# Kernel tuning notes

Measured on AMD Instinct MI355X. Metric: run time of the kernel, lower is better.

The kernel has to match this reference:

```python
import jax, jax.numpy as jnp
import numpy as np

IN_DIM = 50
N_Y = 100
HID = 256
STEPS = 100
BATCH = 16384


def setup_inputs() -> dict:
    key = jax.random.key(0)
    ks = jax.random.split(key, 12)
    def lin(k, out_d, in_d):
        bound = 1.0 / np.sqrt(in_d)
        return jax.random.uniform(k, (out_d, in_d), jnp.float32, -bound, bound)
    def vec(k, out_d, in_d):
        bound = 1.0 / np.sqrt(in_d)
        return jax.random.uniform(k, (out_d,), jnp.float32, -bound, bound)
    return {
        "x": jax.random.normal(ks[0], (BATCH, IN_DIM), jnp.float32),
        "W1": lin(ks[1], 128, IN_DIM), "b1": vec(ks[2], 128, IN_DIM),
        "W2": lin(ks[3], 128, 128), "b2": vec(ks[4], 128, 128),
        "W3": lin(ks[5], HID, 128), "b3": vec(ks[6], HID, 128),
        "Wih": lin(ks[7], 4 * HID, HID), "Whh": lin(ks[8], 4 * HID, HID),
        "bih": vec(ks[9], 4 * HID, HID), "bhh": vec(ks[10], 4 * HID, HID),
        "Wo": lin(ks[11], N_Y, HID),
        "bo": vec(jax.random.fold_in(key, 99), N_Y, HID),
    }


def _forward(x, W1, b1, W2, b2, W3, b3, Wih, Whh, bih, bhh, Wo, bo):
    h = jax.nn.relu(x @ W1.T + b1)
    h = jax.nn.relu(h @ W2.T + b2)
    h = jax.nn.relu(h @ W3.T + b3)  # [B, 256] -> h0 and c0
    # LSTMCell input is h itself, so x@Wih.T + h@Whh.T == h @ (Wih+Whh).T
    Wg = (Wih + Whh).T            # [256, 1024]
    bg = bih + bhh                # [1024]

    def step(carry, _):
        ht, ct = carry
        gates = ht @ Wg + bg                       # [B, 1024]
        i, f, g, o = jnp.split(gates, 4, axis=-1)  # PyTorch gate order i,f,g,o
        i = jax.nn.sigmoid(i)
        f = jax.nn.sigmoid(f)
        g = jnp.tanh(g)
        o = jax.nn.sigmoid(o)
        ct = f * ct + i * g
        ht = o * jnp.tanh(ct)
        y = ht @ Wo.T + bo                         # [B, n_y]
        return (ht, ct), y

    (_, _), ys = jax.lax.scan(step, (h, h), None, length=STEPS)
    return jnp.transpose(ys, (1, 0, 2))  # [B, STEPS, n_y]


def reference(x, W1, b1, W2, b2, W3, b3, Wih, Whh, bih, bhh, Wo, bo):
    return _forward(x, W1, b1, W2, b2, W3, b3, Wih, Whh, bih, bhh, Wo, bo)
```

## Files before the change

### kernel.cpp

```cpp
#include <hip/hip_runtime.h>

#define IN_DIM 50
#define H1 128
#define H2 128
#define HID 256
#define NGATE 1024
#define N_Y 100
#define NYP 128
#define STEPS 100
#define BATCH 16384
#define ROWS 64
#define NTHR 512

typedef float f32x16 __attribute__((ext_vector_type(16)));
typedef __bf16 bf16x8 __attribute__((ext_vector_type(8)));
typedef int i32x4 __attribute__((ext_vector_type(4)));

#define CSTRIDE 264
#define HHI_OFF 0
#define HLO_OFF 33792
#define H2T_OFF 67584
#define SMEM_BYTES 100352

#define WGH_OFF 0
#define WGL_OFF 524288
#define WOH_OFF 1048576
#define WOL_OFF 1114112
#define BG_OFF  1179648
#define BO_OFF  1183744

__device__ __forceinline__ float fast_sigmoid(float x) {
    float e = __expf(-x);
    return __builtin_amdgcn_rcpf(1.0f + e);
}
__device__ __forceinline__ float fast_tanh(float x) {
    float e = __expf(2.0f * x);
    return 1.0f - 2.0f * __builtin_amdgcn_rcpf(1.0f + e);
}
__device__ __forceinline__ unsigned short bf16bits(float x) {
    __bf16 b = (__bf16)x;
    return __builtin_bit_cast(unsigned short, b);
}
__device__ __forceinline__ float bits2f(unsigned short u) {
    __bf16 b = __builtin_bit_cast(__bf16, u);
    return (float)b;
}
__device__ __forceinline__ f32x16 splat16(float v) {
    f32x16 r;
    #pragma unroll
    for (int i = 0; i < 16; ++i) r[i] = v;
    return r;
}

extern "C" __global__ void prep_kernel(const float* __restrict__ Wih,
                                       const float* __restrict__ Whh,
                                       const float* __restrict__ bih,
                                       const float* __restrict__ bhh,
                                       const float* __restrict__ Wo,
                                       const float* __restrict__ bo,
                                       char* __restrict__ ws) {
    int idx = blockIdx.x * blockDim.x + threadIdx.x;
    if (idx < 262144) {
        int n = idx >> 8, k = idx & 255;
        float v = Wih[n * HID + k] + Whh[n * HID + k];
        __bf16 hi = (__bf16)v;
        __bf16 lo = (__bf16)(v - (float)hi);
        int dst = ((n >> 5) * 16 + (k >> 4)) * 512 + ((n & 31) + 32 * ((k >> 3) & 1)) * 8 + (k & 7);
        ((__bf16*)(ws + WGH_OFF))[dst] = hi;
        ((__bf16*)(ws + WGL_OFF))[dst] = lo;
    } else if (idx < 294912) {
        int j = idx - 262144;
        int n = j >> 8, k = j & 255;
        float v = (n < N_Y) ? Wo[n * HID + k] : 0.0f;
        __bf16 hi = (__bf16)v;
        __bf16 lo = (__bf16)(v - (float)hi);
        int dst = ((n >> 5) * 16 + (k >> 4)) * 512 + ((n & 31) + 32 * ((k >> 3) & 1)) * 8 + (k & 7);
        ((__bf16*)(ws + WOH_OFF))[dst] = hi;
        ((__bf16*)(ws + WOL_OFF))[dst] = lo;
    } else if (idx < 295936) {
        int n = idx - 294912;
        ((float*)(ws + BG_OFF))[n] = bih[n] + bhh[n];
    } else if (idx < 296064) {
        int n = idx - 295936;
        ((float*)(ws + BO_OFF))[n] = (n < N_Y) ? bo[n] : 0.0f;
    }
}

extern "C" __global__ void __launch_bounds__(NTHR, 2)
rnn_main(const float* __restrict__ x,
         const float* __restrict__ W1, const float* __restrict__ b1,
         const float* __restrict__ W2, const float* __restrict__ b2,
         const float* __restrict__ W3, const float* __restrict__ b3,
         const char* __restrict__ ws,
         float* __restrict__ out)
{
    __shared__ __align__(16) char smem[SMEM_BYTES];

    const int tid  = threadIdx.x;
    const int lane = tid & 63;
    const int lm   = lane & 31;
    const int l5   = lane >> 5;
    const int w    = __builtin_amdgcn_readfirstlane(tid >> 6);
    const int r0   = blockIdx.x * ROWS;

    {
        float* xt  = (float*)(smem + HHI_OFF);
        float* h1t = (float*)(smem + HLO_OFF);
        float* h2t = (float*)(smem + H2T_OFF);

        for (int i = tid; i < ROWS * IN_DIM; i += NTHR) {
            int r = i / IN_DIM, k = i - r * IN_DIM;
            xt[k * ROWS + r] = x[(size_t)(r0 + r) * IN_DIM + k];
        }
        __syncthreads();

        #pragma unroll
        for (int jt = 0; jt < 2; ++jt) {
            const int jb = w * 16 + jt * 8;
            float acc[8];
            #pragma unroll
            for (int jj = 0; jj < 8; ++jj) acc[jj] = b1[jb + jj];
            for (int k = 0; k < IN_DIM; ++k) {
                float h = xt[k * ROWS + lane];
                #pragma unroll
                for (int jj = 0; jj < 8; ++jj)
                    acc[jj] = fmaf(h, W1[(jb + jj) * IN_DIM + k], acc[jj]);
            }
            #pragma unroll
            for (int jj = 0; jj < 8; ++jj)
                h1t[(jb + jj) * ROWS + lane] = fmaxf(acc[jj], 0.0f);
        }
        __syncthreads();

        #pragma unroll
        for (int jt = 0; jt < 2; ++jt) {
            const int jb = w * 16 + jt * 8;
            float acc[8];
            #pragma unroll
            for (int jj = 0; jj < 8; ++jj) acc[jj] = b2[jb + jj];
            for (int k = 0; k < H1; ++k) {
                float h = h1t[k * ROWS + lane];
                #pragma unroll
                for (int jj = 0; jj < 8; ++jj)
                    acc[jj] = fmaf(h, W2[(jb + jj) * H1 + k], acc[jj]);
            }
            #pragma unroll
            for (int jj = 0; jj < 8; ++jj)
                h2t[(jb + jj) * ROWS + lane] = fmaxf(acc[jj], 0.0f);
        }
        __syncthreads();

        unsigned short* hhi = (unsigned short*)(smem + HHI_OFF);
        unsigned short* hlo = (unsigned short*)(smem + HLO_OFF);
        #pragma unroll
        for (int jt = 0; jt < 4; ++jt) {
            const int jb = w * 32 + jt * 8;
            float acc[8];
            #pragma unroll
            for (int jj = 0; jj < 8; ++jj) acc[jj] = b3[jb + jj];
            for (int k = 0; k < H2; ++k) {
                float h = h2t[k * ROWS + lane];
                #pragma unroll
                for (int jj = 0; jj < 8; ++jj)
                    acc[jj] = fmaf(h, W3[(jb + jj) * H2 + k], acc[jj]);
            }
            #pragma unroll
            for (int jj = 0; jj < 8; ++jj) {
                float v = fmaxf(acc[jj], 0.0f);
                unsigned short hb = bf16bits(v);
                unsigned short lb = bf16bits(v - bits2f(hb));
                hhi[lane * CSTRIDE + jb + jj] = hb;
                hlo[lane * CSTRIDE + jb + jj] = lb;
            }
        }
        __syncthreads();
    }

    const bf16x8* __restrict__ BgH = (const bf16x8*)(ws + WGH_OFF);
    const bf16x8* __restrict__ BgL = (const bf16x8*)(ws + WGL_OFF);
    const bf16x8* __restrict__ BoH = (const bf16x8*)(ws + WOH_OFF);
    const bf16x8* __restrict__ BoL = (const bf16x8*)(ws + WOL_OFF);
    const float*  __restrict__ bg  = (const float*)(ws + BG_OFF);
    const float*  __restrict__ boP = (const float*)(ws + BO_OFF);

    float bgv[4];
    #pragma unroll
    for (int c = 0; c < 4; ++c) bgv[c] = bg[c * 256 + w * 32 + lm];
    const int yct = w & 3, yrt = w >> 2;
    const float bo_v = boP[yct * 32 + lm];

    const int aoff = lm * (CSTRIDE * 2) + l5 * 16;
    const int colb = (w * 32 + lm) * 2;

    float cst[2][16];
    {
        const unsigned short* hhi = (const unsigned short*)(smem + HHI_OFF);
        const unsigned short* hlo = (const unsigned short*)(smem + HLO_OFF);
        #pragma unroll
        for (int rt = 0; rt < 2; ++rt)
            #pragma unroll
            for (int r = 0; r < 16; ++r) {
                int row = rt * 32 + (r & 3) + 8 * (r >> 2) + 4 * l5;
                int cell = w * 32 + lm;
                cst[rt][r] = bits2f(hhi[row * CSTRIDE + cell]) + bits2f(hlo[row * CSTRIDE + cell]);
            }
    }

    for (int t = 0; t < STEPS; ++t) {
        f32x16 acc[4][2];
        #pragma unroll
        for (int c = 0; c < 4; ++c) {
            acc[c][0] = splat16(bgv[c]);
            acc[c][1] = splat16(bgv[c]);
        }

        #pragma unroll 2
        for (int kk = 0; kk < 16; ++kk) {
            const int kb = kk * 32;
            bf16x8 ah0 = __builtin_bit_cast(bf16x8, *(const i32x4*)(smem + HHI_OFF + aoff + kb));
            bf16x8 ah1 = __builtin_bit_cast(bf16x8, *(const i32x4*)(smem + HHI_OFF + 16896 + aoff + kb));
            bf16x8 al0 = __builtin_bit_cast(bf16x8, *(const i32x4*)(smem + HLO_OFF + aoff + kb));
            bf16x8 al1 = __builtin_bit_cast(bf16x8, *(const i32x4*)(smem + HLO_OFF + 16896 + aoff + kb));
            #pragma unroll
            for (int c = 0; c < 4; ++c) {
                const int fb = ((c * 8 + w) * 16 + kk) * 64 + lane;
                bf16x8 bh = BgH[fb];
                bf16x8 bl = BgL[fb];
                acc[c][0] = __builtin_amdgcn_mfma_f32_32x32x16_bf16(ah0, bh, acc[c][0], 0, 0, 0);
                acc[c][1] = __builtin_amdgcn_mfma_f32_32x32x16_bf16(ah1, bh, acc[c][1], 0, 0, 0);
                acc[c][0] = __builtin_amdgcn_mfma_f32_32x32x16_bf16(al0, bh, acc[c][0], 0, 0, 0);
                acc[c][1] = __builtin_amdgcn_mfma_f32_32x32x16_bf16(al1, bh, acc[c][1], 0, 0, 0);
                acc[c][0] = __builtin_amdgcn_mfma_f32_32x32x16_bf16(ah0, bl, acc[c][0], 0, 0, 0);
                acc[c][1] = __builtin_amdgcn_mfma_f32_32x32x16_bf16(ah1, bl, acc[c][1], 0, 0, 0);
            }
        }

        unsigned int hn[2][16];
        #pragma unroll
        for (int rt = 0; rt < 2; ++rt)
            #pragma unroll
            for (int r = 0; r < 16; ++r) {
                float vi = fast_sigmoid(acc[0][rt][r]);
                float vf = fast_sigmoid(acc[1][rt][r]);
                float vg = fast_tanh(acc[2][rt][r]);
                float vo = fast_sigmoid(acc[3][rt][r]);
                float c  = fmaf(vf, cst[rt][r], vi * vg);
                cst[rt][r] = c;
                float h  = vo * fast_tanh(c);
                unsigned short hb = bf16bits(h);
                unsigned short lb = bf16bits(h - bits2f(hb));
                hn[rt][r] = (unsigned int)hb | ((unsigned int)lb << 16);
            }

        __syncthreads();

        #pragma unroll
        for (int rt = 0; rt < 2; ++rt)
            #pragma unroll
            for (int r = 0; r < 16; ++r) {
                int row = rt * 32 + (r & 3) + 8 * (r >> 2) + 4 * l5;
                int ro = row * (CSTRIDE * 2) + colb;
                *(unsigned short*)(smem + HHI_OFF + ro) = (unsigned short)hn[rt][r];
                *(unsigned short*)(smem + HLO_OFF + ro) = (unsigned short)(hn[rt][r] >> 16);
            }

        __syncthreads();

        f32x16 ya = splat16(bo_v);
        const int yao = yrt * 16896 + aoff;
        #pragma unroll 2
        for (int kk = 0; kk < 16; ++kk) {
            const int kb = kk * 32;
            bf16x8 ah = __builtin_bit_cast(bf16x8, *(const i32x4*)(smem + HHI_OFF + yao + kb));
            bf16x8 al = __builtin_bit_cast(bf16x8, *(const i32x4*)(smem + HLO_OFF + yao + kb));
            const int fb = (yct * 16 + kk) * 64 + lane;
            bf16x8 bh = BoH[fb];
            bf16x8 bl = BoL[fb];
            ya = __builtin_amdgcn_mfma_f32_32x32x16_bf16(ah, bh, ya, 0, 0, 0);
            ya = __builtin_amdgcn_mfma_f32_32x32x16_bf16(al, bh, ya, 0, 0, 0);
            ya = __builtin_amdgcn_mfma_f32_32x32x16_bf16(ah, bl, ya, 0, 0, 0);
        }
        const int col = yct * 32 + lm;
        if (col < N_Y) {
            #pragma unroll
            for (int r = 0; r < 16; ++r) {
                int row = yrt * 32 + (r & 3) + 8 * (r >> 2) + 4 * l5;
                out[(size_t)(r0 + row) * (STEPS * N_Y) + t * N_Y + col] = ya[r];
            }
        }
    }
}

extern "C" void kernel_launch(void* const* d_in, const int* in_sizes, int n_in,
                              void* d_out, int out_size, void* d_ws, size_t ws_size,
                              hipStream_t stream) {
    const float* x   = (const float*)d_in[0];
    const float* W1  = (const float*)d_in[1];
    const float* b1  = (const float*)d_in[2];
    const float* W2  = (const float*)d_in[3];
    const float* b2  = (const float*)d_in[4];
    const float* W3  = (const float*)d_in[5];
    const float* b3  = (const float*)d_in[6];
    const float* Wih = (const float*)d_in[7];
    const float* Whh = (const float*)d_in[8];
    const float* bih = (const float*)d_in[9];
    const float* bhh = (const float*)d_in[10];
    const float* Wo  = (const float*)d_in[11];
    const float* bo  = (const float*)d_in[12];
    float* out = (float*)d_out;
    char* ws = (char*)d_ws;

    hipLaunchKernelGGL(prep_kernel, dim3(1157), dim3(256), 0, stream,
                       Wih, Whh, bih, bhh, Wo, bo, ws);
    hipLaunchKernelGGL(rnn_main, dim3(BATCH / ROWS), dim3(NTHR), 0, stream,
                       x, W1, b1, W2, b2, W3, b3, ws, out);
}
```

Baseline: 3.501 ms.

## Split LSTM gate tiles across 16 waves with shared-memory i*g exchange

Doubles the block to 1024 threads so each wave computes two gate tiles instead of four. The lower eight waves compute i and g, store i*g to a new shared-memory exchange buffer, and later run the output projection. The upper eight waves compute f and o, update the cell state and write the new h. The aim is to halve per-wave accumulator registers and MFMA work on the recurrent critical path. In exchange it uses more shared memory (133 KB per block), adds a barrier and a cross-wave data exchange, and leaves half the waves idle during the elementwise update.

```diff
diff --git a/kernel.cpp b/kernel.cpp
--- a/kernel.cpp
+++ b/kernel.cpp
@@ -4,13 +4,11 @@
 #define H1 128
 #define H2 128
 #define HID 256
-#define NGATE 1024
 #define N_Y 100
-#define NYP 128
 #define STEPS 100
 #define BATCH 16384
 #define ROWS 64
-#define NTHR 512
+#define NTHR 1024
 
 typedef float f32x16 __attribute__((ext_vector_type(16)));
 typedef __bf16 bf16x8 __attribute__((ext_vector_type(8)));
@@ -19,8 +17,11 @@
 #define CSTRIDE 264
 #define HHI_OFF 0
 #define HLO_OFF 33792
-#define H2T_OFF 67584
-#define SMEM_BYTES 100352
+#define EXCH_OFF 67584
+#define SMEM_BYTES 133120
+#define H1T_OFF 0
+#define XT_OFF  67584
+#define H2T_OFF 80384
 
 #define WGH_OFF 0
 #define WGL_OFF 524288
@@ -86,7 +87,7 @@
     }
 }
 
-extern "C" __global__ void __launch_bounds__(NTHR, 2)
+extern "C" __global__ void __launch_bounds__(NTHR, 4)
 rnn_main(const float* __restrict__ x,
          const float* __restrict__ W1, const float* __restrict__ b1,
          const float* __restrict__ W2, const float* __restrict__ b2,
@@ -102,10 +103,14 @@
     const int l5   = lane >> 5;
     const int w    = __builtin_amdgcn_readfirstlane(tid >> 6);
     const int r0   = blockIdx.x * ROWS;
+    const bool isLo = (w < 8);
+    const int cb   = w & 7;
+    const int nt0  = (isLo ? 0 : 8) + cb;
+    const int nt1  = nt0 + 16;
 
     {
-        float* xt  = (float*)(smem + HHI_OFF);
-        float* h1t = (float*)(smem + HLO_OFF);
+        float* xt  = (float*)(smem + XT_OFF);
+        float* h1t = (float*)(smem + H1T_OFF);
         float* h2t = (float*)(smem + H2T_OFF);
 
         for (int i = tid; i < ROWS * IN_DIM; i += NTHR) {
@@ -114,47 +119,45 @@
         }
         __syncthreads();
 
+        {
+            const int jb = w * 8;
+            float acc[8];
+            #pragma unroll
+            for (int jj = 0; jj < 8; ++jj) acc[jj] = b1[jb + jj];
+            for (int k = 0; k < IN_DIM; ++k) {
+                float h = xt[k * ROWS + lane];
+                #pragma unroll
+                for (int jj = 0; jj < 8; ++jj)
+                    acc[jj] = fmaf(h, W1[(jb + jj) * IN_DIM + k], acc[jj]);
+            }
+            #pragma unroll
+            for (int jj = 0; jj < 8; ++jj)
+                h1t[(jb + jj) * ROWS + lane] = fmaxf(acc[jj], 0.0f);
+        }
+        __syncthreads();
+
+        {
+            const int jb = w * 8;
+            float acc[8];
+            #pragma unroll
+            for (int jj = 0; jj < 8; ++jj) acc[jj] = b2[jb + jj];
+            for (int k = 0; k < H1; ++k) {
+                float h = h1t[k * ROWS + lane];
+                #pragma unroll
+                for (int jj = 0; jj < 8; ++jj)
+                    acc[jj] = fmaf(h, W2[(jb + jj) * H1 + k], acc[jj]);
+            }
+            #pragma unroll
+            for (int jj = 0; jj < 8; ++jj)
+                h2t[(jb + jj) * ROWS + lane] = fmaxf(acc[jj], 0.0f);
+        }
+        __syncthreads();
+
+        unsigned short* hhi = (unsigned short*)(smem + HHI_OFF);
+        unsigned short* hlo = (unsigned short*)(smem + HLO_OFF);
         #pragma unroll
         for (int jt = 0; jt < 2; ++jt) {
             const int jb = w * 16 + jt * 8;
-            float acc[8];
-            #pragma unroll
-            for (int jj = 0; jj < 8; ++jj) acc[jj] = b1[jb + jj];
-            for (int k = 0; k < IN_DIM; ++k) {
-                float h = xt[k * ROWS + lane];
-                #pragma unroll
-                for (int jj = 0; jj < 8; ++jj)
-                    acc[jj] = fmaf(h, W1[(jb + jj) * IN_DIM + k], acc[jj]);
-            }
-            #pragma unroll
-            for (int jj = 0; jj < 8; ++jj)
-                h1t[(jb + jj) * ROWS + lane] = fmaxf(acc[jj], 0.0f);
-        }
-        __syncthreads();
-
-        #pragma unroll
-        for (int jt = 0; jt < 2; ++jt) {
-            const int jb = w * 16 + jt * 8;
-            float acc[8];
-            #pragma unroll
-            for (int jj = 0; jj < 8; ++jj) acc[jj] = b2[jb + jj];
-            for (int k = 0; k < H1; ++k) {
-                float h = h1t[k * ROWS + lane];
-                #pragma unroll
-                for (int jj = 0; jj < 8; ++jj)
-                    acc[jj] = fmaf(h, W2[(jb + jj) * H1 + k], acc[jj]);
-            }
-            #pragma unroll
-            for (int jj = 0; jj < 8; ++jj)
-                h2t[(jb + jj) * ROWS + lane] = fmaxf(acc[jj], 0.0f);
-        }
-        __syncthreads();
-
-        unsigned short* hhi = (unsigned short*)(smem + HHI_OFF);
-        unsigned short* hlo = (unsigned short*)(smem + HLO_OFF);
-        #pragma unroll
-        for (int jt = 0; jt < 4; ++jt) {
-            const int jb = w * 32 + jt * 8;
             float acc[8];
             #pragma unroll
             for (int jj = 0; jj < 8; ++jj) acc[jj] = b3[jb + jj];
@@ -183,17 +186,18 @@
     const float*  __restrict__ bg  = (const float*)(ws + BG_OFF);
     const float*  __restrict__ boP = (const float*)(ws + BO_OFF);
 
-    float bgv[4];
-    #pragma unroll
-    for (int c = 0; c < 4; ++c) bgv[c] = bg[c * 256 + w * 32 + lm];
-    const int yct = w & 3, yrt = w >> 2;
+    const float bg0 = bg[nt0 * 32 + lm];
+    const float bg1 = bg[nt1 * 32 + lm];
+    const int yrt = w >> 2, yct = w & 3;
     const float bo_v = boP[yct * 32 + lm];
 
     const int aoff = lm * (CSTRIDE * 2) + l5 * 16;
-    const int colb = (w * 32 + lm) * 2;
+    const int colb = (cb * 32 + lm) * 2;
+    float* exch = (float*)(smem + EXCH_OFF);
+    const int exbase = (cb * 2 * 16) * 64 + lane;
 
     float cst[2][16];
-    {
+    if (!isLo) {
         const unsigned short* hhi = (const unsigned short*)(smem + HHI_OFF);
         const unsigned short* hlo = (const unsigned short*)(smem + HLO_OFF);
         #pragma unroll
@@ -201,18 +205,15 @@
             #pragma unroll
             for (int r = 0; r < 16; ++r) {
                 int row = rt * 32 + (r & 3) + 8 * (r >> 2) + 4 * l5;
-                int cell = w * 32 + lm;
+                int cell = cb * 32 + lm;
                 cst[rt][r] = bits2f(hhi[row * CSTRIDE + cell]) + bits2f(hlo[row * CSTRIDE + cell]);
             }
     }
 
     for (int t = 0; t < STEPS; ++t) {
-        f32x16 acc[4][2];
-        #pragma unroll
-        for (int c = 0; c < 4; ++c) {
-            acc[c][0] = splat16(bgv[c]);
-            acc[c][1] = splat16(bgv[c]);
-        }
+        f32x16 g0[2], g1[2];
+        g0[0] = splat16(bg0); g0[1] = splat16(bg0);
+        g1[0] = splat16(bg1); g1[1] = splat16(bg1);
 
         #pragma unroll 2
         for (int kk = 0; kk < 16; ++kk) {
@@ -221,71 +222,78 @@
             bf16x8 ah1 = __builtin_bit_cast(bf16x8, *(const i32x4*)(smem + HHI_OFF + 16896 + aoff + kb));
             bf16x8 al0 = __builtin_bit_cast(bf16x8, *(const i32x4*)(smem + HLO_OFF + aoff + kb));
             bf16x8 al1 = __builtin_bit_cast(bf16x8, *(const i32x4*)(smem + HLO_OFF + 16896 + aoff + kb));
-            #pragma unroll
-            for (int c = 0; c < 4; ++c) {
-                const int fb = ((c * 8 + w) * 16 + kk) * 64 + lane;
-                bf16x8 bh = BgH[fb];
-                bf16x8 bl = BgL[fb];
-                acc[c][0] = __builtin_amdgcn_mfma_f32_32x32x16_bf16(ah0, bh, acc[c][0], 0, 0, 0);
-                acc[c][1] = __builtin_amdgcn_mfma_f32_32x32x16_bf16(ah1, bh, acc[c][1], 0, 0, 0);
-                acc[c][0] = __builtin_amdgcn_mfma_f32_32x32x16_bf16(al0, bh, acc[c][0], 0, 0, 0);
-                acc[c][1] = __builtin_amdgcn_mfma_f32_32x32x16_bf16(al1, bh, acc[c][1], 0, 0, 0);
-                acc[c][0] = __builtin_amdgcn_mfma_f32_32x32x16_bf16(ah0, bl, acc[c][0], 0, 0, 0);
-                acc[c][1] = __builtin_amdgcn_mfma_f32_32x32x16_bf16(ah1, bl, acc[c][1], 0, 0, 0);
-            }
-        }
-
-        unsigned int hn[2][16];
-        #pragma unroll
-        for (int rt = 0; rt < 2; ++rt)
-            #pragma unroll
-            for (int r = 0; r < 16; ++r) {
-                float vi = fast_sigmoid(acc[0][rt][r]);
-                float vf = fast_sigmoid(acc[1][rt][r]);
-                float vg = fast_tanh(acc[2][rt][r]);
-                float vo = fast_sigmoid(acc[3][rt][r]);
-                float c  = fmaf(vf, cst[rt][r], vi * vg);
-                cst[rt][r] = c;
-                float h  = vo * fast_tanh(c);
-                unsigned short hb = bf16bits(h);
-                unsigned short lb = bf16bits(h - bits2f(hb));
-                hn[rt][r] = (unsigned int)hb | ((unsigned int)lb << 16);
-            }
-
-        __syncthreads();
-
-        #pragma unroll
-        for (int rt = 0; rt < 2; ++rt)
-            #pragma unroll
-            for (int r = 0; r < 16; ++r) {
-                int row = rt * 32 + (r & 3) + 8 * (r >> 2) + 4 * l5;
-                int ro = row * (CSTRIDE * 2) + colb;
-                *(unsigned short*)(smem + HHI_OFF + ro) = (unsigned short)hn[rt][r];
-                *(unsigned short*)(smem + HLO_OFF + ro) = (unsigned short)(hn[rt][r] >> 16);
-            }
-
-        __syncthreads();
-
-        f32x16 ya = splat16(bo_v);
-        const int yao = yrt * 16896 + aoff;
-        #pragma unroll 2
-        for (int kk = 0; kk < 16; ++kk) {
-            const int kb = kk * 32;
-            bf16x8 ah = __builtin_bit_cast(bf16x8, *(const i32x4*)(smem + HHI_OFF + yao + kb));
-            bf16x8 al = __builtin_bit_cast(bf16x8, *(const i32x4*)(smem + HLO_OFF + yao + kb));
-            const int fb = (yct * 16 + kk) * 64 + lane;
-            bf16x8 bh = BoH[fb];
-            bf16x8 bl = BoL[fb];
-            ya = __builtin_amdgcn_mfma_f32_32x32x16_bf16(ah, bh, ya, 0, 0, 0);
-            ya = __builtin_amdgcn_mfma_f32_32x32x16_bf16(al, bh, ya, 0, 0, 0);
-            ya = __builtin_amdgcn_mfma_f32_32x32x16_bf16(ah, bl, ya, 0, 0, 0);
-        }
-        const int col = yct * 32 + lm;
-        if (col < N_Y) {
-            #pragma unroll
-            for (int r = 0; r < 16; ++r) {
-                int row = yrt * 32 + (r & 3) + 8 * (r >> 2) + 4 * l5;
-                out[(size_t)(r0 + row) * (STEPS * N_Y) + t * N_Y + col] = ya[r];
+            bf16x8 b0h = BgH[(nt0 * 16 + kk) * 64 + lane];
+            bf16x8 b0l = BgL[(nt0 * 16 + kk) * 64 + lane];
+            bf16x8 b1h = BgH[(nt1 * 16 + kk) * 64 + lane];
+            bf16x8 b1l = BgL[(nt1 * 16 + kk) * 64 + lane];
+            g0[0] = __builtin_amdgcn_mfma_f32_32x32x16_bf16(ah0, b0h, g0[0], 0, 0, 0);
+            g0[1] = __builtin_amdgcn_mfma_f32_32x32x16_bf16(ah1, b0h, g0[1], 0, 0, 0);
+            g0[0] = __builtin_amdgcn_mfma_f32_32x32x16_bf16(al0, b0h, g0[0], 0, 0, 0);
+            g0[1] = __builtin_amdgcn_mfma_f32_32x32x16_bf16(al1, b0h, g0[1], 0, 0, 0);
+            g0[0] = __builtin_amdgcn_mfma_f32_32x32x16_bf16(ah0, b0l, g0[0], 0, 0, 0);
+            g0[1] = __builtin_amdgcn_mfma_f32_32x32x16_bf16(ah1, b0l, g0[1], 0, 0, 0);
+            g1[0] = __builtin_amdgcn_mfma_f32_32x32x16_bf16(ah0, b1h, g1[0], 0, 0, 0);
+            g1[1] = __builtin_amdgcn_mfma_f32_32x32x16_bf16(ah1, b1h, g1[1], 0, 0, 0);
+            g1[0] = __builtin_amdgcn_mfma_f32_32x32x16_bf16(al0, b1h, g1[0], 0, 0, 0);
+            g1[1] = __builtin_amdgcn_mfma_f32_32x32x16_bf16(al1, b1h, g1[1], 0, 0, 0);
+            g1[0] = __builtin_amdgcn_mfma_f32_32x32x16_bf16(ah0, b1l, g1[0], 0, 0, 0);
+            g1[1] = __builtin_amdgcn_mfma_f32_32x32x16_bf16(ah1, b1l, g1[1], 0, 0, 0);
+        }
+
+        if (isLo) {
+            #pragma unroll
+            for (int rt = 0; rt < 2; ++rt)
+                #pragma unroll
+                for (int r = 0; r < 16; ++r)
+                    exch[exbase + rt * 1024 + r * 64] =
+                        fast_sigmoid(g0[rt][r]) * fast_tanh(g1[rt][r]);
+        }
+
+        __syncthreads();
+
+        if (!isLo) {
+            #pragma unroll
+            for (int rt = 0; rt < 2; ++rt)
+                #pragma unroll
+                for (int r = 0; r < 16; ++r) {
+                    float vf = fast_sigmoid(g0[rt][r]);
+                    float vo = fast_sigmoid(g1[rt][r]);
+                    float p  = exch[exbase + rt * 1024 + r * 64];
+                    float c  = fmaf(vf, cst[rt][r], p);
+                    cst[rt][r] = c;
+                    float h  = vo * fast_tanh(c);
+                    unsigned short hb = bf16bits(h);
+                    unsigned short lb = bf16bits(h - bits2f(hb));
+                    int row = rt * 32 + (r & 3) + 8 * (r >> 2) + 4 * l5;
+                    int ro  = row * (CSTRIDE * 2) + colb;
+                    *(unsigned short*)(smem + HHI_OFF + ro) = hb;
+                    *(unsigned short*)(smem + HLO_OFF + ro) = lb;
+                }
+        }
+
+        __syncthreads();
+
+        if (isLo) {
+            f32x16 ya = splat16(bo_v);
+            const int yao = yrt * 16896 + aoff;
+            #pragma unroll 2
+            for (int kk = 0; kk < 16; ++kk) {
+                const int kb = kk * 32;
+                bf16x8 ah = __builtin_bit_cast(bf16x8, *(const i32x4*)(smem + HHI_OFF + yao + kb));
+                bf16x8 al = __builtin_bit_cast(bf16x8, *(const i32x4*)(smem + HLO_OFF + yao + kb));
+                bf16x8 bh = BoH[(yct * 16 + kk) * 64 + lane];
+                bf16x8 bl = BoL[(yct * 16 + kk) * 64 + lane];
+                ya = __builtin_amdgcn_mfma_f32_32x32x16_bf16(ah, bh, ya, 0, 0, 0);
+                ya = __builtin_amdgcn_mfma_f32_32x32x16_bf16(al, bh, ya, 0, 0, 0);
+                ya = __builtin_amdgcn_mfma_f32_32x32x16_bf16(ah, bl, ya, 0, 0, 0);
+            }
+            const int col = yct * 32 + lm;
+            if (col < N_Y) {
+                #pragma unroll
+                for (int r = 0; r < 16; ++r) {
+                    int row = yrt * 32 + (r & 3) + 8 * (r >> 2) + 4 * l5;
+                    out[(size_t)(r0 + row) * (STEPS * N_Y) + t * N_Y + col] = ya[r];
+                }
             }
         }
     }
```

Result: slower. 3.887 ms (+11.0%).
